# Performance work log

Hardware: AMD Instinct MI355X
Metric: run time of the kernel (lower is better)

## Reference

```python
import jax, jax.numpy as jnp
import numpy as np

T, H, I, E, K = 1024, 1024, 512, 32, 4   # tokens, hidden, moe_inter, n_experts, top_k
G, TG, NS = 8, 4, 2                      # n_group, topk_group, n_shared_experts
C = 2 * T * K // E                       # expert capacity (no-drop headroom)
SCALE = 2.5                              # routed_scaling_factor


def setup_inputs() -> dict:
    key = jax.random.key(0)
    ks = jax.random.split(key, 7)
    s = 0.02
    return dict(
        hidden_states=jax.random.normal(ks[0], (T, H), jnp.float32),
        gate_w=jax.random.normal(ks[1], (E, H), jnp.float32) * s,
        e_bias=jax.random.normal(ks[2], (E,), jnp.float32) * 0.1,
        w_gate_up=jax.random.normal(ks[3], (E, 2 * I, H), jnp.float32) * s,
        w_down=jax.random.normal(ks[4], (E, H, I), jnp.float32) * s,
        w_gate_up_shared=jax.random.normal(ks[5], (2 * I * NS, H), jnp.float32) * s,
        w_down_shared=jax.random.normal(ks[6], (H, I * NS), jnp.float32) * s,
    )


def reference(hidden_states, gate_w, e_bias, w_gate_up, w_down, w_gate_up_shared, w_down_shared):
    x = hidden_states                                   # (T, H)
    # --- gate + sigmoid scoring (noaux_tc) ---
    logits = x @ gate_w.T                               # (T, E)
    scores = jax.nn.sigmoid(logits.astype(jnp.float32))
    sfc = scores + e_bias                               # scores_for_choice
    # --- group-limited top-k: top-2 sum per group, keep topk_group groups ---
    group_scores = jax.lax.top_k(sfc.reshape(T, G, E // G), 2)[0].sum(-1)  # (T, G)
    grp_idx = jax.lax.top_k(group_scores, TG)[1]        # (T, TG)
    gmask = jnp.zeros((T, G), jnp.float32).at[jnp.arange(T)[:, None], grp_idx].set(1.0)
    smask = jnp.repeat(gmask, E // G, axis=1)           # (T, E)
    sfc_m = jnp.where(smask > 0, sfc, 0.0)
    topk_idx = jax.lax.top_k(sfc_m, K)[1]               # (T, K)
    tw = jnp.take_along_axis(scores, topk_idx, axis=1)  # weights from raw scores
    tw = tw / (tw.sum(-1, keepdims=True) + 1e-20)       # norm_topk_prob
    tw = tw * SCALE
    # --- capacity-based dispatch (position within expert via cumsum of one-hot) ---
    e_flat = topk_idx.reshape(-1)                       # (T*K,)
    oh = jax.nn.one_hot(e_flat, E, dtype=jnp.float32)   # (T*K, E)
    pos = jnp.sum((jnp.cumsum(oh, axis=0) - 1.0) * oh, axis=-1).astype(jnp.int32)
    keep = (pos < C).astype(jnp.float32)                # capacity sized to never drop
    pos_c = jnp.clip(pos, 0, C - 1)
    t_flat = jnp.repeat(jnp.arange(T), K)
    combine = jnp.zeros((T, E, C), jnp.float32).at[t_flat, e_flat, pos_c].add(tw.reshape(-1) * keep)
    dispatch = jnp.zeros((T, E, C), jnp.float32).at[t_flat, e_flat, pos_c].add(keep)
    # --- grouped expert MLP (gate_up -> SiluAndMul -> down) ---
    xe = jnp.einsum('tec,th->ech', dispatch, x)         # (E, C, H)
    gu = jnp.einsum('ech,eoh->eco', xe, w_gate_up)      # (E, C, 2I)
    act = jax.nn.silu(gu[..., :I]) * gu[..., I:]
    ye = jnp.einsum('eci,ehi->ech', act, w_down)        # (E, C, H)
    routed = jnp.einsum('tec,ech->th', combine, ye)     # (T, H)
    # --- shared experts MLP on residual ---
    IS = I * NS
    gus = x @ w_gate_up_shared.T                        # (T, 2*IS)
    acts = jax.nn.silu(gus[:, :IS]) * gus[:, IS:]
    shared = acts @ w_down_shared.T                     # (T, H)
    return routed + shared
```

## Files before the change

### kernel.cpp

```cpp
#include <hip/hip_runtime.h>
#include <hip/hip_bf16.h>
#include <math.h>

#define T_TOK 1024
#define H_DIM 1024
#define I_DIM 512
#define E_NUM 32
#define K_TOP 4
#define G_NUM 8
#define TG_NUM 4
#define CAP 256
#define IS_DIM 1024
#define RSCALE 2.5f

#define MAXTILES 72

#define WS_CNT_OFF    0
#define WS_NT_OFF     128
#define WS_TILE_OFF   256
#define WS_EIDX_OFF   4096
#define WS_WN_OFF     20480
#define WS_STOK_OFF   36864
#define WS_SW_OFF     69632
#define WS_ACT_OFF    102400
#define WS_ACTS_OFF   (102400 + (size_t)E_NUM*CAP*I_DIM*2)
#define WS_XB_OFF     (WS_ACTS_OFF + (size_t)T_TOK*IS_DIM*2)
#define WS_T2S_OFF    (WS_XB_OFF + (size_t)T_TOK*H_DIM*2)
#define WS_YR_OFF     (WS_T2S_OFF + (size_t)T_TOK*K_TOP*4)

typedef __attribute__((ext_vector_type(8))) short short8v;
typedef __attribute__((ext_vector_type(4))) float f32x4;
typedef __attribute__((ext_vector_type(4))) unsigned uint4v;

__device__ __forceinline__ short f2bf(float f) {
    unsigned u = __float_as_uint(f);
    u += 0x7FFFu + ((u >> 16) & 1u);
    return (short)(u >> 16);
}
__device__ __forceinline__ unsigned pk2bf(float a, float b) {
    unsigned ua = __float_as_uint(a) + 0x8000u;
    unsigned ub = __float_as_uint(b) + 0x8000u;
    return __builtin_amdgcn_perm(ub, ua, 0x07060302);
}
__device__ __forceinline__ uint4v pk8bf(float4 lo, float4 hi) {
    uint4v r; r.x = pk2bf(lo.x, lo.y); r.y = pk2bf(lo.z, lo.w);
    r.z = pk2bf(hi.x, hi.y); r.w = pk2bf(hi.z, hi.w); return r;
}
__device__ __forceinline__ float silu_(float g) { return g / (1.f + expf(-g)); }

#define BAR_RELAXED() do { \
    asm volatile("s_waitcnt lgkmcnt(0)" ::: "memory"); \
    __builtin_amdgcn_s_barrier(); \
    asm volatile("" ::: "memory"); \
} while (0)

#define LDSTRIDE 72

__global__ __launch_bounds__(256) void gate_kernel(
    const float* __restrict__ x, const float* __restrict__ gate_w,
    const float* __restrict__ e_bias,
    int* __restrict__ eidx, float* __restrict__ wnorm, short* __restrict__ xb)
{
    __shared__ float xs[H_DIM];
    __shared__ float logits[E_NUM];
    const int t = blockIdx.x;
    const int tid = threadIdx.x;
    float4 v = ((const float4*)(x + (size_t)t * H_DIM))[tid];
    ((float4*)xs)[tid] = v;
    {
        unsigned* xd = (unsigned*)(xb + (size_t)t * H_DIM) + tid * 2;
        xd[0] = pk2bf(v.x, v.y); xd[1] = pk2bf(v.z, v.w);
    }
    __syncthreads();

    const int e = tid >> 3, sub = tid & 7;
    const float4* gw4 = (const float4*)(gate_w + (size_t)e * H_DIM + sub * 128);
    const float4* xr4 = (const float4*)(xs + sub * 128);
    float p = 0.f;
    #pragma unroll
    for (int h = 0; h < 32; ++h) {
        float4 a = xr4[h], b = gw4[h];
        p += a.x * b.x + a.y * b.y + a.z * b.z + a.w * b.w;
    }
    for (int off = 4; off; off >>= 1) p += __shfl_down(p, off, 8);
    if (sub == 0) logits[e] = p;
    __syncthreads();
    if (tid != 0) return;

    float sc[E_NUM], sfc[E_NUM];
    for (int i = 0; i < E_NUM; ++i) {
        sc[i] = 1.f / (1.f + expf(-logits[i]));
        sfc[i] = sc[i] + e_bias[i];
    }
    float gs[G_NUM];
    for (int g = 0; g < G_NUM; ++g) {
        float m1 = -1e30f, m2 = -1e30f;
        for (int j = 0; j < E_NUM / G_NUM; ++j) {
            float v2 = sfc[g * (E_NUM / G_NUM) + j];
            if (v2 > m1) { m2 = m1; m1 = v2; } else if (v2 > m2) m2 = v2;
        }
        gs[g] = m1 + m2;
    }
    bool gm[G_NUM];
    for (int g = 0; g < G_NUM; ++g) gm[g] = false;
    for (int it = 0; it < TG_NUM; ++it) {
        int best = -1; float bv = -1e30f;
        for (int g = 0; g < G_NUM; ++g) if (!gm[g] && gs[g] > bv) { bv = gs[g]; best = g; }
        gm[best] = true;
    }
    float sm[E_NUM];
    for (int i = 0; i < E_NUM; ++i) sm[i] = gm[i / (E_NUM / G_NUM)] ? sfc[i] : 0.0f;
    int idx[K_TOP]; float w[K_TOP]; float tsum = 0.f;
    for (int it = 0; it < K_TOP; ++it) {
        int best = 0; float bv = -1e30f;
        for (int i = 0; i < E_NUM; ++i) if (sm[i] > bv) { bv = sm[i]; best = i; }
        sm[best] = -1e30f;
        idx[it] = best; w[it] = sc[best]; tsum += w[it];
    }
    float inv = RSCALE / (tsum + 1e-20f);
    const int base = t * K_TOP;
    for (int it = 0; it < K_TOP; ++it) {
        eidx[base + it] = idx[it];
        wnorm[base + it] = w[it] * inv;
    }
}

__global__ __launch_bounds__(256) void assign_kernel(
    const int* __restrict__ eidx, const float* __restrict__ wnorm,
    int* __restrict__ cnt, int* __restrict__ slot_token, float* __restrict__ slot_w,
    int* __restrict__ ntiles, int* __restrict__ tiles, int* __restrict__ tok2slot)
{
    __shared__ int   se[T_TOK * K_TOP];
    __shared__ float swt[T_TOK * K_TOP];
    __shared__ int   scnt[E_NUM];
    const int tid = threadIdx.x;
    for (int i = tid; i < T_TOK * K_TOP; i += 256) { se[i] = eidx[i]; swt[i] = wnorm[i]; }
    __syncthreads();

    const int e = tid >> 3;
    const int seg = tid & 7;
    const int base = seg * 512;
    int c = 0;
    for (int i = 0; i < 512; ++i) c += (se[base + i] == e);
    int excl = 0, total = 0;
    for (int s = 0; s < 8; ++s) {
        int cs = __shfl(c, s, 8);
        total += cs;
        if (s < seg) excl += cs;
    }
    if (seg == 0) { cnt[e] = total; scnt[e] = total; }
    __syncthreads();
    int boff = 0;
    for (int ee = 0; ee < e; ++ee) boff += min(scnt[ee], CAP);

    int pos = excl;
    for (int i = 0; i < 512; ++i) {
        if (se[base + i] == e) {
            const int g = base + i;
            if (pos < CAP) {
                slot_token[e * CAP + pos] = g >> 2;
                slot_w[e * CAP + pos] = swt[g];
                tok2slot[g] = boff + pos;
            } else {
                tok2slot[g] = -1;
            }
            ++pos;
        }
    }
    __syncthreads();
    if (tid == 0) {
        int nt = 0;
        for (int t0 = 0; t0 < T_TOK; t0 += 128) {
            tiles[nt * 4] = -1; tiles[nt * 4 + 1] = t0; tiles[nt * 4 + 2] = 128;
            tiles[nt * 4 + 3] = 0; ++nt;
        }
        int off = 0;
        for (int ee = 0; ee < E_NUM; ++ee) {
            int n = min(scnt[ee], CAP);
            for (int r = 0; r < n; r += 128) {
                tiles[nt * 4] = ee; tiles[nt * 4 + 1] = r;
                tiles[nt * 4 + 2] = min(128, n - r);
                tiles[nt * 4 + 3] = off + r; ++nt;
            }
            off += n;
        }
        *ntiles = nt;
    }
}


#define GEMM_SETUP() \
    const int tid = threadIdx.x; \
    const int lane = tid & 63, wid = tid >> 6; \
    const int wm = wid & 1, wn = wid >> 1; \
    const int lr16 = lane & 15, kc = lane >> 4; \
    const int sc_ = tid & 7, srow = tid >> 3; \
    const int aoff0 = srow * LDSTRIDE + sc_ * 8; \
    const int aoff1 = (srow + 64) * LDSTRIDE + sc_ * 8;

#define DECL_ACC42() f32x4 acc[4][2]; \
    _Pragma("unroll") for (int i_ = 0; i_ < 4; ++i_) \
    _Pragma("unroll") for (int j_ = 0; j_ < 2; ++j_) acc[i_][j_] = 0.f;

#define COMPUTE_BK64(Asb, Bsb) do { \
    _Pragma("unroll") for (int ks = 0; ks < 2; ++ks) { \
        short8v a_[4], b_[2]; \
        _Pragma("unroll") for (int mt = 0; mt < 4; ++mt) \
            a_[mt] = *(const short8v*)&(Asb)[(wm*64 + mt*16 + lr16)*LDSTRIDE + ks*32 + kc*8]; \
        _Pragma("unroll") for (int nt = 0; nt < 2; ++nt) \
            b_[nt] = *(const short8v*)&(Bsb)[(wn*32 + nt*16 + lr16)*LDSTRIDE + ks*32 + kc*8]; \
        _Pragma("unroll") for (int mt = 0; mt < 4; ++mt) \
        _Pragma("unroll") for (int nt = 0; nt < 2; ++nt) \
            acc[mt][nt] = __builtin_amdgcn_mfma_f32_16x16x32_bf16(a_[mt], b_[nt], acc[mt][nt], 0, 0, 0); \
    } \
} while (0)

__global__ __launch_bounds__(512, 4) void gu_all_kernel(
    const short* __restrict__ xb, const float* __restrict__ w_gate_up,
    const float* __restrict__ w_gus,
    const int* __restrict__ ntiles, const int* __restrict__ tiles,
    const int* __restrict__ slot_token, const float* __restrict__ slot_w,
    short* __restrict__ act, short* __restrict__ acts)
{
    if ((int)blockIdx.y >= *ntiles) return;
    const int e  = tiles[blockIdx.y * 4];
    const int r0 = tiles[blockIdx.y * 4 + 1];
    const int ne = tiles[blockIdx.y * 4 + 2];
    const bool sh = (e < 0);
    if (!sh && blockIdx.x >= I_DIM / 64) return;
    const int col0 = blockIdx.x * 64;

    __shared__ __align__(16) short As[2][128 * LDSTRIDE];
    __shared__ __align__(16) short Bs[2][128 * LDSTRIDE];
    __shared__ int   toks[128];
    __shared__ float sws[128];

    GEMM_SETUP();
    if (tid < 128) {
        if (sh) { toks[tid] = r0 + tid; sws[tid] = 1.f; }
        else {
            bool v = tid < ne;
            toks[tid] = v ? slot_token[e * CAP + r0 + tid] : 0;
            sws[tid]  = v ? slot_w[e * CAP + r0 + tid] : 0.f;
        }
    }
    __syncthreads();

    const int IDim = sh ? IS_DIM : I_DIM;
    const float* wbase = sh ? w_gus : (w_gate_up + (size_t)e * (2 * I_DIM) * H_DIM);
    const int r_0 = srow, r_1 = srow + 64;
    const int wr0 = ((r_0 >> 4) & 1) * IDim + col0 + ((r_0 >> 5) << 4) + (r_0 & 15);
    const int wr1 = ((r_1 >> 4) & 1) * IDim + col0 + ((r_1 >> 5) << 4) + (r_1 & 15);
    const float* bptr0 = wbase + (size_t)wr0 * H_DIM + sc_ * 8;
    const float* bptr1 = wbase + (size_t)wr1 * H_DIM + sc_ * 8;
    const short* aptr0 = xb + (size_t)toks[r_0] * H_DIM + sc_ * 8;
    const short* aptr1 = xb + (size_t)toks[r_1] * H_DIM + sc_ * 8;

    DECL_ACC42();
    short8v cA0 = *(const short8v*)(aptr0), cA1 = *(const short8v*)(aptr1);
    float4 cB0a = *(const float4*)(bptr0), cB0b = *(const float4*)(bptr0 + 4);
    float4 cB1a = *(const float4*)(bptr1), cB1b = *(const float4*)(bptr1 + 4);

    int buf = 0;
    for (int k0 = 0; k0 < H_DIM; k0 += 64) {
        short8v nA0{}, nA1{};
        float4 nB0a{}, nB0b{}, nB1a{}, nB1b{};
        const int k1 = k0 + 64;
        if (k1 < H_DIM) {
            nA0 = *(const short8v*)(aptr0 + k1);  nA1 = *(const short8v*)(aptr1 + k1);
            nB0a = *(const float4*)(bptr0 + k1);  nB0b = *(const float4*)(bptr0 + k1 + 4);
            nB1a = *(const float4*)(bptr1 + k1);  nB1b = *(const float4*)(bptr1 + k1 + 4);
        }
        *(short8v*)&As[buf][aoff0] = cA0;
        *(short8v*)&As[buf][aoff1] = cA1;
        *(uint4v*)&Bs[buf][aoff0]  = pk8bf(cB0a, cB0b);
        *(uint4v*)&Bs[buf][aoff1]  = pk8bf(cB1a, cB1b);
        BAR_RELAXED();
        COMPUTE_BK64(As[buf], Bs[buf]);
        buf ^= 1;
        cA0 = nA0; cA1 = nA1;
        cB0a = nB0a; cB0b = nB0b; cB1a = nB1a; cB1b = nB1b;
    }

    #pragma unroll
    for (int mt = 0; mt < 4; ++mt) {
        f32x4 g = acc[mt][0], u = acc[mt][1];
        const int colI = col0 + wn * 16 + lr16;
        #pragma unroll
        for (int i = 0; i < 4; ++i) {
            int r = wm * 64 + mt * 16 + kc * 4 + i;
            if (r < ne) {
                float s = sws[r];
                short* dst = sh ? (acts + (size_t)(r0 + r) * IS_DIM + colI)
                                : (act + ((size_t)e * CAP + r0 + r) * I_DIM + colI);
                *dst = f2bf(s * silu_(g[i]) * u[i]);
            }
        }
    }
}

__global__ __launch_bounds__(512, 4) void down_all_kernel(
    const short* __restrict__ act, const short* __restrict__ acts,
    const float* __restrict__ w_down, const float* __restrict__ w_ds,
    const int* __restrict__ ntiles, const int* __restrict__ tiles,
    float* __restrict__ yr, float* __restrict__ out)
{
    if ((int)blockIdx.y >= *ntiles) return;
    const int e  = tiles[blockIdx.y * 4];
    const int r0 = tiles[blockIdx.y * 4 + 1];
    const int ne = tiles[blockIdx.y * 4 + 2];
    const int bo = tiles[blockIdx.y * 4 + 3];
    const bool sh = (e < 0);
    const int h0 = blockIdx.x * 128;

    __shared__ __align__(16) short As[2][128 * LDSTRIDE];
    __shared__ __align__(16) short Bs[2][128 * LDSTRIDE];

    GEMM_SETUP();

    const int Kdim = sh ? IS_DIM : I_DIM;
    const short* abase = sh ? (acts + (size_t)r0 * IS_DIM)
                            : (act + ((size_t)e * CAP + r0) * I_DIM);
    const float* wbase = sh ? w_ds : (w_down + (size_t)e * H_DIM * I_DIM);
    const float* bptr0 = wbase + (size_t)(h0 + srow) * Kdim + sc_ * 8;
    const float* bptr1 = wbase + (size_t)(h0 + srow + 64) * Kdim + sc_ * 8;
    const short* aptr0 = abase + (size_t)srow * Kdim + sc_ * 8;
    const short* aptr1 = abase + (size_t)(srow + 64) * Kdim + sc_ * 8;

    DECL_ACC42();
    short8v cA0 = *(const short8v*)(aptr0), cA1 = *(const short8v*)(aptr1);
    float4 cB0a = *(const float4*)(bptr0), cB0b = *(const float4*)(bptr0 + 4);
    float4 cB1a = *(const float4*)(bptr1), cB1b = *(const float4*)(bptr1 + 4);

    int buf = 0;
    for (int k0 = 0; k0 < Kdim; k0 += 64) {
        short8v nA0{}, nA1{};
        float4 nB0a{}, nB0b{}, nB1a{}, nB1b{};
        const int k1 = k0 + 64;
        if (k1 < Kdim) {
            nA0 = *(const short8v*)(aptr0 + k1);  nA1 = *(const short8v*)(aptr1 + k1);
            nB0a = *(const float4*)(bptr0 + k1);  nB0b = *(const float4*)(bptr0 + k1 + 4);
            nB1a = *(const float4*)(bptr1 + k1);  nB1b = *(const float4*)(bptr1 + k1 + 4);
        }
        *(short8v*)&As[buf][aoff0] = cA0;
        *(short8v*)&As[buf][aoff1] = cA1;
        *(uint4v*)&Bs[buf][aoff0]  = pk8bf(cB0a, cB0b);
        *(uint4v*)&Bs[buf][aoff1]  = pk8bf(cB1a, cB1b);
        BAR_RELAXED();
        COMPUTE_BK64(As[buf], Bs[buf]);
        buf ^= 1;
        cA0 = nA0; cA1 = nA1;
        cB0a = nB0a; cB0b = nB0b; cB1a = nB1a; cB1b = nB1b;
    }

    #pragma unroll
    for (int mt = 0; mt < 4; ++mt) {
        #pragma unroll
        for (int i = 0; i < 4; ++i) {
            int r = wm * 64 + mt * 16 + kc * 4 + i;
            if (r < ne) {
                float* orow = sh ? (out + (size_t)(r0 + r) * H_DIM + h0 + wn * 32)
                                 : (yr + (size_t)(bo + r) * H_DIM + h0 + wn * 32);
                #pragma unroll
                for (int nt = 0; nt < 2; ++nt)
                    orow[nt * 16 + lr16] = acc[mt][nt][i];
            }
        }
    }
}

__global__ __launch_bounds__(256) void combine_kernel(
    const float* __restrict__ yr, const int* __restrict__ tok2slot,
    float* __restrict__ out)
{
    const int t = blockIdx.x, tid = threadIdx.x;
    float4 a = ((const float4*)(out + (size_t)t * H_DIM))[tid];
    #pragma unroll
    for (int k = 0; k < K_TOP; ++k) {
        int s = tok2slot[t * K_TOP + k];
        if (s >= 0) {
            float4 b = ((const float4*)(yr + (size_t)s * H_DIM))[tid];
            a.x += b.x; a.y += b.y; a.z += b.z; a.w += b.w;
        }
    }
    ((float4*)(out + (size_t)t * H_DIM))[tid] = a;
}

extern "C" void kernel_launch(void* const* d_in, const int* in_sizes, int n_in,
                              void* d_out, int out_size, void* d_ws, size_t ws_size,
                              hipStream_t stream) {
    const float* x   = (const float*)d_in[0];
    const float* gw  = (const float*)d_in[1];
    const float* eb  = (const float*)d_in[2];
    const float* wgu = (const float*)d_in[3];
    const float* wd  = (const float*)d_in[4];
    const float* wgs = (const float*)d_in[5];
    const float* wds = (const float*)d_in[6];
    float* out = (float*)d_out;
    char* ws = (char*)d_ws;

    int*   cnt    = (int*)(ws + WS_CNT_OFF);
    int*   ntiles = (int*)(ws + WS_NT_OFF);
    int*   tiles  = (int*)(ws + WS_TILE_OFF);
    int*   eidx   = (int*)(ws + WS_EIDX_OFF);
    float* wnorm  = (float*)(ws + WS_WN_OFF);
    int*   stok   = (int*)(ws + WS_STOK_OFF);
    float* sw     = (float*)(ws + WS_SW_OFF);
    short* act    = (short*)(ws + WS_ACT_OFF);
    short* acts   = (short*)(ws + WS_ACTS_OFF);
    short* xb     = (short*)(ws + WS_XB_OFF);
    int*   t2s    = (int*)(ws + WS_T2S_OFF);
    float* yr     = (float*)(ws + WS_YR_OFF);

    gate_kernel<<<T_TOK, 256, 0, stream>>>(x, gw, eb, eidx, wnorm, xb);
    assign_kernel<<<1, 256, 0, stream>>>(eidx, wnorm, cnt, stok, sw, ntiles, tiles, t2s);
    gu_all_kernel<<<dim3(IS_DIM / 64, MAXTILES), 512, 0, stream>>>(
        xb, wgu, wgs, ntiles, tiles, stok, sw, act, acts);
    down_all_kernel<<<dim3(H_DIM / 128, MAXTILES), 512, 0, stream>>>(
        act, acts, wd, wds, ntiles, tiles, yr, out);
    combine_kernel<<<T_TOK, 256, 0, stream>>>(yr, t2s, out);
}
```

Before: 400.5 us.

## Deepen GEMM global-load prefetch to two stages and widen assign kernel to 1024 threads

The gate-up and down GEMM main loops now keep two register-staged K-slices in flight, loading the slice two steps ahead while computing the current one. The goal is to hide more global-load latency behind the MFMA work. The single-block assign kernel now runs 1024 threads, with 32 segments per expert instead of 8, which shortens its serial counting and scatter loops. The cost is more live registers under launch bounds of 512 threads and 4 blocks, so the compiler may spill or cut occupancy.

```diff
diff --git a/kernel.cpp b/kernel.cpp
--- a/kernel.cpp
+++ b/kernel.cpp
@@ -125,7 +125,7 @@
     }
 }
 
-__global__ __launch_bounds__(256) void assign_kernel(
+__global__ __launch_bounds__(1024) void assign_kernel(
     const int* __restrict__ eidx, const float* __restrict__ wnorm,
     int* __restrict__ cnt, int* __restrict__ slot_token, float* __restrict__ slot_w,
     int* __restrict__ ntiles, int* __restrict__ tiles, int* __restrict__ tok2slot)
@@ -134,17 +134,17 @@
     __shared__ float swt[T_TOK * K_TOP];
     __shared__ int   scnt[E_NUM];
     const int tid = threadIdx.x;
-    for (int i = tid; i < T_TOK * K_TOP; i += 256) { se[i] = eidx[i]; swt[i] = wnorm[i]; }
-    __syncthreads();
-
-    const int e = tid >> 3;
-    const int seg = tid & 7;
-    const int base = seg * 512;
+    for (int i = tid; i < T_TOK * K_TOP; i += 1024) { se[i] = eidx[i]; swt[i] = wnorm[i]; }
+    __syncthreads();
+
+    const int e = tid >> 5;
+    const int seg = tid & 31;
+    const int base = seg * 128;
     int c = 0;
-    for (int i = 0; i < 512; ++i) c += (se[base + i] == e);
+    for (int i = 0; i < 128; ++i) c += (se[base + i] == e);
     int excl = 0, total = 0;
-    for (int s = 0; s < 8; ++s) {
-        int cs = __shfl(c, s, 8);
+    for (int s = 0; s < 32; ++s) {
+        int cs = __shfl(c, s, 32);
         total += cs;
         if (s < seg) excl += cs;
     }
@@ -154,7 +154,7 @@
     for (int ee = 0; ee < e; ++ee) boff += min(scnt[ee], CAP);
 
     int pos = excl;
-    for (int i = 0; i < 512; ++i) {
+    for (int i = 0; i < 128; ++i) {
         if (se[base + i] == e) {
             const int g = base + i;
             if (pos < CAP) {
@@ -214,6 +214,39 @@
             acc[mt][nt] = __builtin_amdgcn_mfma_f32_16x16x32_bf16(a_[mt], b_[nt], acc[mt][nt], 0, 0, 0); \
     } \
 } while (0)
+
+#define LOAD_SET(A0, A1, B0a, B0b, B1a, B1b, KOFF) do { \
+    A0 = *(const short8v*)(aptr0 + (KOFF)); \
+    A1 = *(const short8v*)(aptr1 + (KOFF)); \
+    B0a = *(const float4*)(bptr0 + (KOFF)); B0b = *(const float4*)(bptr0 + (KOFF) + 4); \
+    B1a = *(const float4*)(bptr1 + (KOFF)); B1b = *(const float4*)(bptr1 + (KOFF) + 4); \
+} while (0)
+
+#define STAGE_SET(A0, A1, B0a, B0b, B1a, B1b, BUF) do { \
+    *(short8v*)&As[BUF][aoff0] = A0; \
+    *(short8v*)&As[BUF][aoff1] = A1; \
+    *(uint4v*)&Bs[BUF][aoff0]  = pk8bf(B0a, B0b); \
+    *(uint4v*)&Bs[BUF][aoff1]  = pk8bf(B1a, B1b); \
+} while (0)
+
+#define PIPE_BODY(KDIM) \
+    short8v pA0, pA1, qA0, qA1; \
+    float4 pB0a, pB0b, pB1a, pB1b, qB0a, qB0b, qB1a, qB1b; \
+    LOAD_SET(pA0, pA1, pB0a, pB0b, pB1a, pB1b, 0); \
+    LOAD_SET(qA0, qA1, qB0a, qB0b, qB1a, qB1b, 64); \
+    int buf = 0; \
+    for (int k0 = 0; k0 < (KDIM); k0 += 128) { \
+        STAGE_SET(pA0, pA1, pB0a, pB0b, pB1a, pB1b, buf); \
+        if (k0 + 128 < (KDIM)) LOAD_SET(pA0, pA1, pB0a, pB0b, pB1a, pB1b, k0 + 128); \
+        BAR_RELAXED(); \
+        COMPUTE_BK64(As[buf], Bs[buf]); \
+        buf ^= 1; \
+        STAGE_SET(qA0, qA1, qB0a, qB0b, qB1a, qB1b, buf); \
+        if (k0 + 192 < (KDIM)) LOAD_SET(qA0, qA1, qB0a, qB0b, qB1a, qB1b, k0 + 192); \
+        BAR_RELAXED(); \
+        COMPUTE_BK64(As[buf], Bs[buf]); \
+        buf ^= 1; \
+    }
 
 __global__ __launch_bounds__(512, 4) void gu_all_kernel(
     const short* __restrict__ xb, const float* __restrict__ w_gate_up,
@@ -257,30 +290,7 @@
     const short* aptr1 = xb + (size_t)toks[r_1] * H_DIM + sc_ * 8;
 
     DECL_ACC42();
-    short8v cA0 = *(const short8v*)(aptr0), cA1 = *(const short8v*)(aptr1);
-    float4 cB0a = *(const float4*)(bptr0), cB0b = *(const float4*)(bptr0 + 4);
-    float4 cB1a = *(const float4*)(bptr1), cB1b = *(const float4*)(bptr1 + 4);
-
-    int buf = 0;
-    for (int k0 = 0; k0 < H_DIM; k0 += 64) {
-        short8v nA0{}, nA1{};
-        float4 nB0a{}, nB0b{}, nB1a{}, nB1b{};
-        const int k1 = k0 + 64;
-        if (k1 < H_DIM) {
-            nA0 = *(const short8v*)(aptr0 + k1);  nA1 = *(const short8v*)(aptr1 + k1);
-            nB0a = *(const float4*)(bptr0 + k1);  nB0b = *(const float4*)(bptr0 + k1 + 4);
-            nB1a = *(const float4*)(bptr1 + k1);  nB1b = *(const float4*)(bptr1 + k1 + 4);
-        }
-        *(short8v*)&As[buf][aoff0] = cA0;
-        *(short8v*)&As[buf][aoff1] = cA1;
-        *(uint4v*)&Bs[buf][aoff0]  = pk8bf(cB0a, cB0b);
-        *(uint4v*)&Bs[buf][aoff1]  = pk8bf(cB1a, cB1b);
-        BAR_RELAXED();
-        COMPUTE_BK64(As[buf], Bs[buf]);
-        buf ^= 1;
-        cA0 = nA0; cA1 = nA1;
-        cB0a = nB0a; cB0b = nB0b; cB1a = nB1a; cB1b = nB1b;
-    }
+    PIPE_BODY(H_DIM);
 
     #pragma unroll
     for (int mt = 0; mt < 4; ++mt) {
@@ -328,30 +338,7 @@
     const short* aptr1 = abase + (size_t)(srow + 64) * Kdim + sc_ * 8;
 
     DECL_ACC42();
-    short8v cA0 = *(const short8v*)(aptr0), cA1 = *(const short8v*)(aptr1);
-    float4 cB0a = *(const float4*)(bptr0), cB0b = *(const float4*)(bptr0 + 4);
-    float4 cB1a = *(const float4*)(bptr1), cB1b = *(const float4*)(bptr1 + 4);
-
-    int buf = 0;
-    for (int k0 = 0; k0 < Kdim; k0 += 64) {
-        short8v nA0{}, nA1{};
-        float4 nB0a{}, nB0b{}, nB1a{}, nB1b{};
-        const int k1 = k0 + 64;
-        if (k1 < Kdim) {
-            nA0 = *(const short8v*)(aptr0 + k1);  nA1 = *(const short8v*)(aptr1 + k1);
-            nB0a = *(const float4*)(bptr0 + k1);  nB0b = *(const float4*)(bptr0 + k1 + 4);
-            nB1a = *(const float4*)(bptr1 + k1);  nB1b = *(const float4*)(bptr1 + k1 + 4);
-        }
-        *(short8v*)&As[buf][aoff0] = cA0;
-        *(short8v*)&As[buf][aoff1] = cA1;
-        *(uint4v*)&Bs[buf][aoff0]  = pk8bf(cB0a, cB0b);
-        *(uint4v*)&Bs[buf][aoff1]  = pk8bf(cB1a, cB1b);
-        BAR_RELAXED();
-        COMPUTE_BK64(As[buf], Bs[buf]);
-        buf ^= 1;
-        cA0 = nA0; cA1 = nA1;
-        cB0a = nB0a; cB0b = nB0b; cB1a = nB1a; cB1b = nB1b;
-    }
+    PIPE_BODY(Kdim);
 
     #pragma unroll
     for (int mt = 0; mt < 4; ++mt) {
@@ -413,7 +400,7 @@
     float* yr     = (float*)(ws + WS_YR_OFF);
 
     gate_kernel<<<T_TOK, 256, 0, stream>>>(x, gw, eb, eidx, wnorm, xb);
-    assign_kernel<<<1, 256, 0, stream>>>(eidx, wnorm, cnt, stok, sw, ntiles, tiles, t2s);
+    assign_kernel<<<1, 1024, 0, stream>>>(eidx, wnorm, cnt, stok, sw, ntiles, tiles, t2s);
     gu_all_kernel<<<dim3(IS_DIM / 64, MAXTILES), 512, 0, stream>>>(
         xb, wgu, wgs, ntiles, tiles, stok, sw, act, acts);
     down_all_kernel<<<dim3(H_DIM / 128, MAXTILES), 512, 0, stream>>>(
```

Measured after the change: 472.5 us. 18.0% more time.
